# Optimization experiments

Hardware: AMD Instinct MI355X
Metric: run time of the kernel (lower is better)

Reference implementation:

```python
import jax, jax.numpy as jnp
import numpy as np
import math

DEPTH = 12
LAMBDA_INIT = 0.8 - 0.6 * math.exp(-0.3 * DEPTH)
EPS = 1e-5


def setup_inputs() -> dict:
    key = jax.random.key(0)
    ks = jax.random.split(key, 10)
    B, S, E, H, D = 2, 2048, 1024, 8, 64
    query = jax.random.normal(ks[0], (B, S, E), dtype=jnp.float32)
    init = 0.02
    Wq = jax.random.normal(ks[1], (E, 2 * H * D), dtype=jnp.float32) * init
    Wk = jax.random.normal(ks[2], (E, 2 * H * D), dtype=jnp.float32) * init
    Wv = jax.random.normal(ks[3], (E, 2 * H * D), dtype=jnp.float32) * init
    Wo = jax.random.normal(ks[4], (2 * H * D, E), dtype=jnp.float32) * init
    lq1 = jax.random.normal(ks[5], (D,), dtype=jnp.float32) * 0.1
    lk1 = jax.random.normal(ks[6], (D,), dtype=jnp.float32) * 0.1
    lq2 = jax.random.normal(ks[7], (D,), dtype=jnp.float32) * 0.1
    lk2 = jax.random.normal(ks[8], (D,), dtype=jnp.float32) * 0.1
    subln_w = jnp.ones((2 * D,), dtype=jnp.float32)
    return {"query": query, "Wq": Wq, "Wk": Wk, "Wv": Wv, "Wo": Wo,
            "lq1": lq1, "lk1": lk1, "lq2": lq2, "lk2": lk2, "subln_w": subln_w}


def reference(query, Wq, Wk, Wv, Wo, lq1, lk1, lq2, lk2, subln_w):
    B, S, E = query.shape
    D = lq1.shape[0]
    H = Wq.shape[1] // (2 * D)
    scaling = D ** -0.5
    # projections -> (B, 2H, S, D) for q/k, (B, H, S, 2D) for v
    q = (query @ Wq).reshape(B, S, 2 * H, D).transpose(0, 2, 1, 3) * scaling
    k = (query @ Wk).reshape(B, S, 2 * H, D).transpose(0, 2, 1, 3)
    v = (query @ Wv).reshape(B, S, H, 2 * D).transpose(0, 2, 1, 3)
    score = jnp.einsum('bhqd,bhkd->bhqk', q, k)  # (B, 2H, S, S)
    score = jnp.nan_to_num(score)
    score = jax.nn.softmax(score.astype(jnp.float32), axis=-1).astype(score.dtype)
    lambda_1 = jnp.exp(jnp.sum(lq1 * lk1))
    lambda_2 = jnp.exp(jnp.sum(lq2 * lk2))
    lambda_full = lambda_1 - lambda_2 + LAMBDA_INIT
    score = score.reshape(B, H, 2, S, S)
    score = score[:, :, 0] - lambda_full * score[:, :, 1]  # (B, H, S, S)
    attn = jnp.einsum('bhqk,bhkd->bhqd', score, v)  # (B, H, S, 2D)
    # RMSNorm over last dim (computed in fp32, cast back), affine weight
    af = attn.astype(jnp.float32)
    attn = (af * jax.lax.rsqrt(jnp.mean(af * af, axis=-1, keepdims=True) + EPS)).astype(attn.dtype)
    attn = attn * subln_w
    attn = attn * (1.0 - LAMBDA_INIT)
    attn = attn.transpose(0, 2, 1, 3).reshape(B, S, H * 2 * D)
    return attn @ Wo
```

## Files before the change

### kernel.cpp

```cpp
#include <hip/hip_runtime.h>

typedef __attribute__((ext_vector_type(4))) float f32x4;
typedef __attribute__((ext_vector_type(8))) short bf16x8;
typedef unsigned short u16;
typedef unsigned int u32;

#define LAMBDA_INIT 0.7836057665311429f
#define ONE_MINUS_LI 0.2163942334688571f
#define QSCALE_LOG2 0.1803368801111137f

__device__ __forceinline__ u16 f2b(float f){
  union { float f; unsigned u; } v; v.f = f;
  unsigned r = v.u + 0x7fff + ((v.u >> 16) & 1);
  return (u16)(r >> 16);
}

__device__ __forceinline__ f32x4 mfma16(bf16x8 a, bf16x8 b, f32x4 c){
  return __builtin_amdgcn_mfma_f32_16x16x32_bf16(a, b, c, 0, 0, 0);
}

__device__ __forceinline__ float exp2_raw(float x){
  float r;
  asm("v_exp_f32 %0, %1" : "=v"(r) : "v"(x));
  return r;
}

__device__ __forceinline__ void async16(void* lds, const void* g){
  __builtin_amdgcn_global_load_lds((const __attribute__((address_space(1))) void*)g,
                                   (__attribute__((address_space(3))) void*)lds, 16, 0, 0);
}

__global__ void prep(const float* __restrict__ query,
                     const float* __restrict__ Wq, const float* __restrict__ Wk,
                     const float* __restrict__ Wv, const float* __restrict__ Wo,
                     u16* __restrict__ Xbf, u16* __restrict__ Wqkvt, u16* __restrict__ Wot){
  int z = blockIdx.z;
  int c0 = blockIdx.x * 32, r0 = blockIdx.y * 32;
  int tx = threadIdx.x, ty = threadIdx.y;
  if (z == 4){
    #pragma unroll
    for (int k = 0; k < 4; k++){
      size_t base = (size_t)(k * 1024 + r0) * 1024;
      for (int i = 0; i < 32; i += 8)
        Xbf[base + (size_t)(ty + i) * 1024 + c0 + tx] =
            f2b(query[base + (size_t)(ty + i) * 1024 + c0 + tx]);
    }
    return;
  }
  __shared__ float t[32][33];
  const float* in = (z == 0) ? Wq : (z == 1) ? Wk : (z == 2) ? Wv : Wo;
  u16* out = (z < 3) ? (Wqkvt + (size_t)z * 1048576) : Wot;
  for (int i = 0; i < 32; i += 8) t[ty + i][tx] = in[(size_t)(r0 + ty + i) * 1024 + c0 + tx];
  __syncthreads();
  for (int i = 0; i < 32; i += 8) out[(size_t)(c0 + ty + i) * 1024 + r0 + tx] = f2b(t[tx][ty + i]);
}

template<int PERM>
__global__ void transpose_bf16(const u16* __restrict__ in, u16* __restrict__ out, int R, int C){
  __shared__ u16 t[32][34];
  int c0 = blockIdx.x * 32, r0 = blockIdx.y * 32;
  size_t boff = (size_t)blockIdx.z * R * C;
  int tx = threadIdx.x, ty = threadIdx.y;
  for (int i = 0; i < 32; i += 8) t[ty + i][tx] = in[boff + (size_t)(r0 + ty + i) * C + c0 + tx];
  __syncthreads();
  for (int i = 0; i < 32; i += 8){
    int dv = c0 + ty + i, s = r0 + tx;
    int sx;
    if (PERM){
      int sl = s & 63;
      int n = sl >> 4, g = (sl >> 2) & 3, r = sl & 3;
      int pos = (s & ~63) | ((n >> 1) << 5) | (g << 3) | ((n & 1) << 2) | r;
      sx = (pos & ~63) | ((((pos >> 3) & 7) ^ (dv & 7)) << 3) | (pos & 7);
    } else sx = s;
    out[boff + (size_t)dv * R + sx] = t[tx][ty + i];
  }
}

template<int BN, int EPI>
__global__ __launch_bounds__(256, 2) void gemm_async(
    const u16* __restrict__ A, const u16* __restrict__ Bt, float* __restrict__ Cp,
    u16* __restrict__ Qo, u16* __restrict__ Ko, u16* __restrict__ Vo,
    int M, int N, int K, int gm){
  constexpr int BCH = BN / 32;
  __shared__ u16 As[2][128 * 64];
  __shared__ u16 Bs[2][BN * 64];
  int tid = threadIdx.x, w = tid >> 6, lane = tid & 63;
  int l16 = lane & 15, grp = lane >> 4;
  int wr = w >> 1, wc = w & 1;
  int nwg = gridDim.x, bid = blockIdx.x;
  int idx = (bid & 7) * (nwg >> 3) + (bid >> 3);
  int m0 = (idx & (gm - 1)) * 128, n0 = (idx / gm) * BN;

  int sr = lane >> 3;
  int sc = ((lane & 7) ^ sr) << 3;
  const u16* pA = A  + (size_t)(m0 + w * 8 + sr) * K + sc;
  const u16* pB = Bt + (size_t)(n0 + w * 8 + sr) * K + sc;

  f32x4 acc[4][BN / 32] = {};

#define STAGEG(bb, k0) do{                                             \
    _Pragma("unroll")                                                  \
    for (int i = 0; i < 4; i++)                                        \
      async16(&As[bb][i * 2048 + w * 512], pA + (k0) + (size_t)i * 32 * K); \
    _Pragma("unroll")                                                  \
    for (int i = 0; i < BCH; i++)                                      \
      async16(&Bs[bb][i * 2048 + w * 512], pB + (k0) + (size_t)i * 32 * K); \
  } while(0)

  STAGEG(0, 0);
  int niter = K >> 6;
  for (int kt = 0; kt < niter; kt++){
    int cur = kt & 1;
    if (kt < niter - 1){
      STAGEG(cur ^ 1, (kt + 1) << 6);
      if constexpr (BN == 128) asm volatile("s_waitcnt vmcnt(8)" ::: "memory");
      else                     asm volatile("s_waitcnt vmcnt(6)" ::: "memory");
    } else {
      asm volatile("s_waitcnt vmcnt(0)" ::: "memory");
    }
    __builtin_amdgcn_s_barrier();

    const u16* Ap = As[cur];
    const u16* Bp = Bs[cur];
    #pragma unroll
    for (int kk = 0; kk < 2; kk++){
      bf16x8 a[4], b[BN / 32];
      #pragma unroll
      for (int m = 0; m < 4; m++){
        int r = wr * 64 + m * 16 + l16;
        a[m] = *(const bf16x8*)&Ap[r * 64 + (((kk * 4 + grp) ^ (r & 7)) << 3)];
      }
      #pragma unroll
      for (int n = 0; n < BCH; n++){
        int r = wc * (BN / 2) + n * 16 + l16;
        b[n] = *(const bf16x8*)&Bp[r * 64 + (((kk * 4 + grp) ^ (r & 7)) << 3)];
      }
      #pragma unroll
      for (int m = 0; m < 4; m++)
        #pragma unroll
        for (int n = 0; n < BCH; n++)
          acc[m][n] = mfma16(a[m], b[n], acc[m][n]);
    }
    if (kt < niter - 1){
      asm volatile("s_waitcnt lgkmcnt(0)" ::: "memory");
      __builtin_amdgcn_s_barrier();
    }
  }
#undef STAGEG

  if constexpr (EPI == 0){
    #pragma unroll
    for (int m = 0; m < 4; m++)
      #pragma unroll
      for (int n = 0; n < BCH; n++)
        #pragma unroll
        for (int r = 0; r < 4; r++)
          Cp[(size_t)(m0 + wr * 64 + m * 16 + grp * 4 + r) * N + n0 + wc * (BN / 2) + n * 16 + l16]
            = acc[m][n][r];
  } else {
    int proj = n0 >> 10;
    #pragma unroll
    for (int m = 0; m < 4; m++){
      int row = m0 + wr * 64 + m * 16 + grp * 4;
      #pragma unroll
      for (int n = 0; n < BCH; n++){
        int col = n0 + wc * (BN / 2) + n * 16 + l16;
        int cn = col & 1023;
        if (proj == 0){
          #pragma unroll
          for (int r = 0; r < 4; r++)
            Qo[(size_t)(row + r) * 1024 + cn] = f2b(acc[m][n][r] * QSCALE_LOG2);
        } else if (proj == 1){
          #pragma unroll
          for (int r = 0; r < 4; r++){
            int cs = (cn & ~63) | ((((cn >> 3) & 7) ^ ((row + r) & 7)) << 3) | (cn & 7);
            Ko[(size_t)(row + r) * 1024 + cs] = f2b(acc[m][n][r]);
          }
        } else {
          #pragma unroll
          for (int r = 0; r < 4; r++)
            Vo[(size_t)(row + r) * 1024 + cn] = f2b(acc[m][n][r]);
        }
      }
    }
  }
}

__global__ __launch_bounds__(256, 2) void diff_attn(
    const u16* __restrict__ Qb, const u16* __restrict__ Kb, const u16* __restrict__ Vt,
    const float* __restrict__ lq1, const float* __restrict__ lk1,
    const float* __restrict__ lq2, const float* __restrict__ lk2,
    const float* __restrict__ slw, u16* __restrict__ attnb){
  __shared__ u16 Ksh[2][2][64 * 64];
  __shared__ u16 Vsh[3][128 * 64];

  int tid = threadIdx.x, w = tid >> 6, lane = tid & 63;
  int l16 = lane & 15, grp = lane >> 4;
  int bid = blockIdx.x;
  int h = bid & 7, qt = (bid >> 3) & 31, b = bid >> 8;
  int tb = b * 2048 + qt * 64;

  float lam;
  {
    float p1 = lq1[lane] * lk1[lane], p2 = lq2[lane] * lk2[lane];
    #pragma unroll
    for (int m = 32; m >= 1; m >>= 1){ p1 += __shfl_xor(p1, m); p2 += __shfl_xor(p2, m); }
    lam = __expf(p1) - __expf(p2) + LAMBDA_INIT;
  }

  const u16* gK1 = Kb + (size_t)(b * 2048 + w * 16 + (lane >> 3)) * 1024 + 128 * h + (lane & 7) * 8;
  const u16* gK2 = gK1 + 64;
  const u16* gV  = Vt + (size_t)(b * 1024 + 128 * h + w * 32 + (lane >> 3)) * 2048 + (lane & 7) * 8;

  bf16x8 q1[2], q2[2];
  {
    const u16* qr = Qb + (size_t)(tb + w * 16 + l16) * 1024 + 128 * h;
    q1[0] = *(const bf16x8*)(qr + grp * 8);
    q1[1] = *(const bf16x8*)(qr + 32 + grp * 8);
    q2[0] = *(const bf16x8*)(qr + 64 + grp * 8);
    q2[1] = *(const bf16x8*)(qr + 96 + grp * 8);
  }

  bf16x8 ones;
  #pragma unroll
  for (int i = 0; i < 8; i++) ones[i] = (short)0x3F80;

#define STAGE_K(bb, PK1, PK2) do{                           \
    async16(&Ksh[bb][0][w * 1024],       (PK1));            \
    async16(&Ksh[bb][0][w * 1024 + 512], (PK1) + 8192);     \
    async16(&Ksh[bb][1][w * 1024],       (PK2));            \
    async16(&Ksh[bb][1][w * 1024 + 512], (PK2) + 8192);     \
  } while(0)
#define STAGE_V(ss, PV) do{                                 \
    async16(&Vsh[ss][w * 2048],          (PV));             \
    async16(&Vsh[ss][w * 2048 + 512],    (PV) + 16384);     \
    async16(&Vsh[ss][w * 2048 + 1024],   (PV) + 32768);     \
    async16(&Vsh[ss][w * 2048 + 1536],   (PV) + 49152);     \
  } while(0)

  int xo0 = ((grp ^ (l16 & 7)) << 3);
  int xo1 = (((4 + grp) ^ (l16 & 7)) << 3);

#define QKCOMP(bb, S1, S2) do{                                           \
    const u16* K1p = Ksh[bb][0];                                         \
    const u16* K2p = Ksh[bb][1];                                         \
    _Pragma("unroll")                                                    \
    for (int n = 0; n < 4; n++){ S1[n] = (f32x4){0,0,0,0}; S2[n] = (f32x4){0,0,0,0}; } \
    _Pragma("unroll")                                                    \
    for (int n = 0; n < 4; n++){                                         \
      int rb = (n * 16 + l16) << 6;                                      \
      bf16x8 k1a = *(const bf16x8*)&K1p[rb + xo0];                       \
      bf16x8 k1b = *(const bf16x8*)&K1p[rb + xo1];                       \
      bf16x8 k2a = *(const bf16x8*)&K2p[rb + xo0];                       \
      bf16x8 k2b = *(const bf16x8*)&K2p[rb + xo1];                       \
      S1[n] = mfma16(k1a, q1[0], S1[n]);                                 \
      S1[n] = mfma16(k1b, q1[1], S1[n]);                                 \
      S2[n] = mfma16(k2a, q2[0], S2[n]);                                 \
      S2[n] = mfma16(k2b, q2[1], S2[n]);                                 \
    }                                                                    \
  } while(0)

#define EXPPACK(S, PB) do{                                               \
    float p[16];                                                         \
    _Pragma("unroll")                                                    \
    for (int n = 0; n < 4; n++)                                          \
      _Pragma("unroll")                                                  \
      for (int r = 0; r < 4; r++) p[n * 4 + r] = exp2_raw(S[n][r] - 4.0f); \
    union { u32 wd[4]; bf16x8 v; } u0, u1;                               \
    _Pragma("unroll")                                                    \
    for (int j = 0; j < 4; j++){                                         \
      asm("v_cvt_pk_bf16_f32 %0, %1, %2" : "=v"(u0.wd[j]) : "v"(p[2 * j]),     "v"(p[2 * j + 1])); \
      asm("v_cvt_pk_bf16_f32 %0, %1, %2" : "=v"(u1.wd[j]) : "v"(p[8 + 2 * j]), "v"(p[9 + 2 * j])); \
    }                                                                    \
    PB[0] = u0.v; PB[1] = u1.v;                                          \
  } while(0)

  STAGE_K(0, gK1, gK2); STAGE_V(0, gV);
  gK1 += 65536; gK2 += 65536; gV += 64;
  STAGE_K(1, gK1, gK2); STAGE_V(1, gV);
  gK1 += 65536; gK2 += 65536; gV += 64;
  __syncthreads();

  f32x4 s1c[4], s2c[4], s1n[4], s2n[4];
  QKCOMP(0, s1c, s2c);
  __syncthreads();

  f32x4 O1[9] = {}, O2[9] = {};
  int vc = 0, vnx = 2;

  for (int kt = 0; kt < 32; kt++){
    int kc = kt & 1;
    if (kt < 30){
      STAGE_K(kc, gK1, gK2);
      STAGE_V(vnx, gV);
      gK1 += 65536; gK2 += 65536; gV += 64;
      asm volatile("s_waitcnt vmcnt(8)" ::: "memory");
    } else if (kt == 30){
      asm volatile("s_waitcnt vmcnt(4)" ::: "memory");
    } else {
      asm volatile("s_waitcnt vmcnt(0)" ::: "memory");
    }
    __builtin_amdgcn_s_barrier();

    if (kt < 31) QKCOMP(kc ^ 1, s1n, s2n);
    bf16x8 pbA[2], pbB[2];
    EXPPACK(s1c, pbA);
    EXPPACK(s2c, pbB);

    const u16* Vp = Vsh[vc];
    __builtin_amdgcn_s_setprio(1);
    #pragma unroll
    for (int kk = 0; kk < 2; kk++){
      int xo = kk ? xo1 : xo0;
      #pragma unroll
      for (int n = 0; n < 8; n++){
        bf16x8 av = *(const bf16x8*)&Vp[((n * 16 + l16) << 6) + xo];
        O1[n] = mfma16(av, pbA[kk], O1[n]);
        O2[n] = mfma16(av, pbB[kk], O2[n]);
      }
      O1[8] = mfma16(ones, pbA[kk], O1[8]);
      O2[8] = mfma16(ones, pbB[kk], O2[8]);
    }
    __builtin_amdgcn_s_setprio(0);

    if (kt < 31){
      asm volatile("s_waitcnt lgkmcnt(0)" ::: "memory");
      __builtin_amdgcn_s_barrier();
      #pragma unroll
      for (int n = 0; n < 4; n++){ s1c[n] = s1n[n]; s2c[n] = s2n[n]; }
    }
    vc = (vc == 2) ? 0 : vc + 1;
    vnx = (vnx == 2) ? 0 : vnx + 1;
  }
#undef STAGE_K
#undef STAGE_V
#undef QKCOMP
#undef EXPPACK

  float i1 = 1.f / O1[8][0], i2 = lam / O2[8][0];
  float x[8][4], ss = 0.f;
  #pragma unroll
  for (int n = 0; n < 8; n++)
    #pragma unroll
    for (int r = 0; r < 4; r++){
      float v = O1[n][r] * i1 - O2[n][r] * i2;
      x[n][r] = v; ss += v * v;
    }
  ss += __shfl_xor(ss, 16);
  ss += __shfl_xor(ss, 32);
  float ri = rsqrtf(ss * (1.f / 128.f) + 1e-5f);
  int row = tb + w * 16 + l16;
  #pragma unroll
  for (int n = 0; n < 8; n++){
    float4 sw = *(const float4*)&slw[n * 16 + grp * 4];
    ushort4 o;
    o.x = f2b(x[n][0] * ri * sw.x * ONE_MINUS_LI);
    o.y = f2b(x[n][1] * ri * sw.y * ONE_MINUS_LI);
    o.z = f2b(x[n][2] * ri * sw.z * ONE_MINUS_LI);
    o.w = f2b(x[n][3] * ri * sw.w * ONE_MINUS_LI);
    *(ushort4*)&attnb[(size_t)row * 1024 + h * 128 + n * 16 + grp * 4] = o;
  }
}

extern "C" void kernel_launch(void* const* d_in, const int* in_sizes, int n_in,
                              void* d_out, int out_size, void* d_ws, size_t ws_size,
                              hipStream_t stream){
  const float* query = (const float*)d_in[0];
  const float* Wq = (const float*)d_in[1];
  const float* Wk = (const float*)d_in[2];
  const float* Wv = (const float*)d_in[3];
  const float* Wo = (const float*)d_in[4];
  const float* lq1 = (const float*)d_in[5];
  const float* lk1 = (const float*)d_in[6];
  const float* lq2 = (const float*)d_in[7];
  const float* lk2 = (const float*)d_in[8];
  const float* slw = (const float*)d_in[9];

  char* ws = (char*)d_ws;
  u16* Xbf   = (u16*)(ws + 0);
  u16* Wqkvt = (u16*)(ws + 8388608);
  u16* Wot   = (u16*)(ws + 14680064);
  u16* Qbuf  = (u16*)(ws + 16777216);
  u16* Kbuf  = (u16*)(ws + 25165824);
  u16* Vbuf  = (u16*)(ws + 33554432);
  u16* Vtr   = (u16*)(ws + 41943040);
  u16* Attn  = (u16*)(ws + 50331648);

  prep<<<dim3(32, 32, 5), dim3(32, 8), 0, stream>>>(query, Wq, Wk, Wv, Wo,
                                                    Xbf, Wqkvt, Wot);

  gemm_async<128, 1><<<768, 256, 0, stream>>>(Xbf, Wqkvt, nullptr, Qbuf, Kbuf, Vbuf,
                                              4096, 3072, 1024, 32);

  transpose_bf16<1><<<dim3(32, 64, 2), dim3(32, 8), 0, stream>>>(Vbuf, Vtr, 2048, 1024);

  diff_attn<<<512, 256, 0, stream>>>(Qbuf, Kbuf, Vtr, lq1, lk1, lq2, lk2, slw, Attn);

  gemm_async<64, 0><<<512, 256, 0, stream>>>(Attn, Wot, (float*)d_out,
                                             nullptr, nullptr, nullptr,
                                             4096, 1024, 1024, 32);
}
```

Before: 132.5 us.

## Merge per-iteration barriers in attention loop and vectorize query bf16 cast

The attention main loop now waits and synchronizes once at the top of each iteration instead of twice (before QK compute and after PV). The staging of the next K/V tiles is issued after that barrier. Separately, the query fp32-to-bf16 conversion in the prep kernel uses float4 loads and ushort4 stores instead of scalar accesses. Dropping a barrier per iteration cuts synchronization stalls, but it depends on the new wait counts and buffer reuse order still protecting the shared-memory tiles from being overwritten early.

```diff
diff --git a/kernel.cpp b/kernel.cpp
--- a/kernel.cpp
+++ b/kernel.cpp
@@ -35,19 +35,23 @@
                      const float* __restrict__ Wv, const float* __restrict__ Wo,
                      u16* __restrict__ Xbf, u16* __restrict__ Wqkvt, u16* __restrict__ Wot){
   int z = blockIdx.z;
-  int c0 = blockIdx.x * 32, r0 = blockIdx.y * 32;
   int tx = threadIdx.x, ty = threadIdx.y;
   if (z == 4){
+    int bidf = blockIdx.y * 32 + blockIdx.x;
+    int t = ty * 32 + tx;
+    const float4* in4 = (const float4*)query;
+    ushort4* out4 = (ushort4*)Xbf;
     #pragma unroll
     for (int k = 0; k < 4; k++){
-      size_t base = (size_t)(k * 1024 + r0) * 1024;
-      for (int i = 0; i < 32; i += 8)
-        Xbf[base + (size_t)(ty + i) * 1024 + c0 + tx] =
-            f2b(query[base + (size_t)(ty + i) * 1024 + c0 + tx]);
+      int i = bidf * 1024 + k * 256 + t;
+      float4 f = in4[i];
+      ushort4 o; o.x = f2b(f.x); o.y = f2b(f.y); o.z = f2b(f.z); o.w = f2b(f.w);
+      out4[i] = o;
     }
     return;
   }
   __shared__ float t[32][33];
+  int c0 = blockIdx.x * 32, r0 = blockIdx.y * 32;
   const float* in = (z == 0) ? Wq : (z == 1) ? Wk : (z == 2) ? Wv : Wo;
   u16* out = (z < 3) ? (Wqkvt + (size_t)z * 1048576) : Wot;
   for (int i = 0; i < 32; i += 8) t[ty + i][tx] = in[(size_t)(r0 + ty + i) * 1024 + c0 + tx];
@@ -280,34 +284,29 @@
   STAGE_K(1, gK1, gK2); STAGE_V(1, gV);
   gK1 += 65536; gK2 += 65536; gV += 64;
   __syncthreads();
-
   f32x4 s1c[4], s2c[4], s1n[4], s2n[4];
   QKCOMP(0, s1c, s2c);
-  __syncthreads();
 
   f32x4 O1[9] = {}, O2[9] = {};
-  int vc = 0, vnx = 2;
+  int vrd = 0, vst = 2;
 
   for (int kt = 0; kt < 32; kt++){
-    int kc = kt & 1;
+    if (kt <= 30) asm volatile("s_waitcnt vmcnt(4) lgkmcnt(0)" ::: "memory");
+    else          asm volatile("s_waitcnt vmcnt(0) lgkmcnt(0)" ::: "memory");
+    __builtin_amdgcn_s_barrier();
+
     if (kt < 30){
-      STAGE_K(kc, gK1, gK2);
-      STAGE_V(vnx, gV);
+      STAGE_K(kt & 1, gK1, gK2);
+      STAGE_V(vst, gV);
       gK1 += 65536; gK2 += 65536; gV += 64;
-      asm volatile("s_waitcnt vmcnt(8)" ::: "memory");
-    } else if (kt == 30){
-      asm volatile("s_waitcnt vmcnt(4)" ::: "memory");
-    } else {
-      asm volatile("s_waitcnt vmcnt(0)" ::: "memory");
-    }
-    __builtin_amdgcn_s_barrier();
-
-    if (kt < 31) QKCOMP(kc ^ 1, s1n, s2n);
+    }
+
+    if (kt < 31) QKCOMP((kt & 1) ^ 1, s1n, s2n);
     bf16x8 pbA[2], pbB[2];
     EXPPACK(s1c, pbA);
     EXPPACK(s2c, pbB);
 
-    const u16* Vp = Vsh[vc];
+    const u16* Vp = Vsh[vrd];
     __builtin_amdgcn_s_setprio(1);
     #pragma unroll
     for (int kk = 0; kk < 2; kk++){
@@ -323,14 +322,10 @@
     }
     __builtin_amdgcn_s_setprio(0);
 
-    if (kt < 31){
-      asm volatile("s_waitcnt lgkmcnt(0)" ::: "memory");
-      __builtin_amdgcn_s_barrier();
-      #pragma unroll
-      for (int n = 0; n < 4; n++){ s1c[n] = s1n[n]; s2c[n] = s2n[n]; }
-    }
-    vc = (vc == 2) ? 0 : vc + 1;
-    vnx = (vnx == 2) ? 0 : vnx + 1;
+    #pragma unroll
+    for (int n = 0; n < 4; n++){ s1c[n] = s1n[n]; s2c[n] = s2n[n]; }
+    vrd = (vrd == 2) ? 0 : vrd + 1;
+    vst = (vst == 2) ? 0 : vst + 1;
   }
 #undef STAGE_K
 #undef STAGE_V
```

Result: no change. 131.1 us (-1.0%).
